# Optimization experiments

Measured on AMD Instinct MI355X. Metric: run time of the kernel, lower is better.

## Reference

```python
import jax, jax.numpy as jnp
import numpy as np

B, S, H, K = 32, 128, 512, 8  # batch, max_sentence_size, hidden_size, cross_share_k


def setup_inputs() -> dict:
    key = jax.random.key(0)
    ks = jax.random.split(key, 6)
    return {
        "aspect_hidden": jax.random.normal(ks[0], (B, S, H), jnp.float32),
        "polarity_hidden": jax.random.normal(ks[1], (B, S, H), jnp.float32),
        "G_aspect_polarity": jax.random.normal(ks[2], (H, K, H), jnp.float32) * 0.05,
        "G_polarity_aspect": jax.random.normal(ks[3], (H, K, H), jnp.float32) * 0.05,
        "G_vector_aspect": jax.random.normal(ks[4], (K, 1), jnp.float32),
        "G_vector_polarity": jax.random.normal(ks[5], (K, 1), jnp.float32),
    }


def _bilinear_score(left, G, right, v):
    # left:[B,S,H], G:[H,K,H], right:[B,T,H], v:[K,1] -> score:[B,S,T]
    # proj[b,s,k,g] = sum_h left[b,s,h] G[h,k,g]
    proj = jnp.einsum('bsh,hkg->bskg', left, G)
    # raw[b,s,t,k] = tanh(sum_g proj[b,s,k,g] right[b,t,g])  (matches source's
    # reshape->matmul->transpose chain)
    raw = jnp.tanh(jnp.einsum('bskg,btg->bstk', proj, right))
    return jnp.einsum('bstk,k->bst', raw, v[:, 0])


def reference(aspect_hidden, polarity_hidden, G_aspect_polarity,
              G_polarity_aspect, G_vector_aspect, G_vector_polarity):
    # Aspect branch: aspect x G_ap x polarity
    aspect_vector = _bilinear_score(aspect_hidden, G_aspect_polarity,
                                    polarity_hidden, G_vector_aspect)
    # Polarity branch: NOTE source uses aspect_hidden on BOTH sides (faithful)
    polarity_vector = _bilinear_score(aspect_hidden, G_polarity_aspect,
                                      aspect_hidden, G_vector_polarity)

    aspect_attn = jax.nn.softmax(aspect_vector, axis=-1)     # [B,S,S]
    polarity_attn = jax.nn.softmax(polarity_vector, axis=-1)  # [B,S,S]

    aspect_out = aspect_hidden + jnp.einsum('bst,bth->bsh', aspect_attn, polarity_hidden)
    polarity_out = polarity_hidden + jnp.einsum('bst,bth->bsh', polarity_attn, aspect_hidden)
    return (aspect_out, polarity_out)
```

## Files before the change

### kernel.cpp

```cpp
#include <hip/hip_runtime.h>

#define BB 32
#define SS 128
#define HH 512
#define KC 8
#define NN 4096

typedef __attribute__((ext_vector_type(8))) short bf16x8;
typedef __attribute__((ext_vector_type(8))) _Float16 f16x8;
typedef __attribute__((ext_vector_type(4))) float f32x4;

__device__ __forceinline__ unsigned short f2bf(float f) {
  unsigned int u = __float_as_uint(f);
  u += 0x7fffu + ((u >> 16) & 1u);
  return (unsigned short)(u >> 16);
}
__device__ __forceinline__ float bf2f(unsigned short h) {
  return __uint_as_float(((unsigned int)h) << 16);
}
__device__ __forceinline__ unsigned short f2fp16(float f) {
  union { _Float16 h; unsigned short u; } cv;
  cv.h = (_Float16)f;
  return cv.u;
}
__device__ __forceinline__ float tanh_fast(float x) {
  float e = __expf(2.0f * x);
  return 1.0f - 2.0f / (e + 1.0f);
}
__device__ __forceinline__ void async16(const void* g, void* lds) {
  __builtin_amdgcn_global_load_lds(
      (const __attribute__((address_space(1))) unsigned int*)g,
      (__attribute__((address_space(3))) unsigned int*)lds, 16, 0, 0);
}

__global__ __launch_bounds__(256) void convert_all(
    const float* __restrict__ Xa, const float* __restrict__ Xb,
    unsigned short* __restrict__ hia, unsigned short* __restrict__ loa,
    unsigned short* __restrict__ hiTa,
    unsigned short* __restrict__ hib, unsigned short* __restrict__ lob,
    unsigned short* __restrict__ hiTb,
    unsigned short* __restrict__ af16,
    const float* __restrict__ Ga, const float* __restrict__ Gb,
    unsigned short* __restrict__ g1f, unsigned short* __restrict__ g2f) {
  __shared__ float t[32][33];
  const int idx = blockIdx.x;
  const int tx = threadIdx.x & 31, ty = threadIdx.x >> 5;
  if (idx < 4096) {
    const int z = idx >> 11, rem = idx & 2047;
    const int h0 = (rem & 15) * 32;
    const int y = rem >> 4;
    const int s0 = (y & 3) * 32;
    const size_t b = y >> 2;
    const float* X = z ? Xb : Xa;
    unsigned short* hi = z ? hib : hia;
    unsigned short* lo = z ? lob : loa;
    unsigned short* hiT = z ? hiTb : hiTa;
#pragma unroll
    for (int r = 0; r < 4; ++r) {
      float f = X[b * (SS * HH) + (size_t)(s0 + ty + r * 8) * HH + h0 + tx];
      t[ty + r * 8][tx] = f;
      size_t o = b * (SS * HH) + (size_t)(s0 + ty + r * 8) * HH + h0 + tx;
      unsigned short h = f2bf(f);
      hi[o] = h;
      lo[o] = f2bf(f - bf2f(h));
      if (!z) af16[o] = f2fp16(f);
    }
    __syncthreads();
#pragma unroll
    for (int r = 0; r < 4; ++r) {
      float f = t[tx][ty + r * 8];
      size_t o = b * (SS * HH) + (size_t)(h0 + ty + r * 8) * SS + s0 + tx;
      hiT[o] = f2fp16(f);
    }
  } else {
    const int j = idx - 4096;
    const int z = j >> 11, rem = j & 2047;
    const int bx = (rem & 127) * 32;
    const int by = (rem >> 7) * 32;
    const float* G = z ? Gb : Ga;
    unsigned short* gf = z ? g2f : g1f;
#pragma unroll
    for (int r = 0; r < 4; ++r)
      t[ty + r * 8][tx] = G[(size_t)(by + ty + r * 8) * NN + bx + tx];
    __syncthreads();
#pragma unroll
    for (int r = 0; r < 4; ++r) {
      float f = t[tx][ty + r * 8];
      size_t o = (size_t)(bx + ty + r * 8) * HH + by + tx;
      gf[o] = f2fp16(f);
    }
  }
}

__global__ __launch_bounds__(256, 2) void fused_score(
    const unsigned short* __restrict__ Ahi, const unsigned short* __restrict__ Alo,
    const unsigned short* __restrict__ Phi, const unsigned short* __restrict__ Plo,
    const unsigned short* __restrict__ Af16,
    const unsigned short* __restrict__ G1f, const unsigned short* __restrict__ G2f,
    const float* __restrict__ v1, const float* __restrict__ v2,
    float* __restrict__ scoreBuf, int bc) {
  __shared__ __align__(16) char smem[65536];
  const int k = blockIdx.x;
  const int b = blockIdx.y;
  const int brx = blockIdx.z;
  const int tid = threadIdx.x, w = tid >> 6, L = tid & 63;
  const int wm = w >> 1, wn = w & 1;
  const int q = L >> 4, c = L & 15;

  const unsigned short* Af = Af16 + (size_t)b * SS * HH;
  const unsigned short* Gf = brx ? G2f : G1f;
  const unsigned short* Rh = (brx ? Ahi : Phi) + (size_t)b * SS * HH;
  const unsigned short* Rl = (brx ? Alo : Plo) + (size_t)b * SS * HH;

  const int rrA = L >> 3;
  const int scA = ((L & 7) ^ rrA) * 8;
  const unsigned short* pAf = Af + (size_t)(w * 32 + rrA) * HH + scA;
  const unsigned short* pGf = Gf + (size_t)(w * 32 + rrA) * HH + scA;

  const int srow = w * 32 + (L >> 2);
  const int slotS = ((L & 3) ^ ((L >> 3) & 3)) * 8;
  const unsigned short* pRh = Rh + (size_t)srow * HH + slotS;
  const unsigned short* pRl = Rl + (size_t)srow * HH + slotS;
  const unsigned lbase = (unsigned)w * 2048;

  const int xr = ((L & 15) >> 1) & 3;
  const int rslot = ((q ^ xr) << 4);
  const int arB = (wm * 64 + (L & 15)) * 64 + rslot;
  const int brB = (wn * 64 + (L & 15)) * 64 + rslot;

  f32x4 raw[4][4];
#pragma unroll
  for (int i = 0; i < 4; ++i)
#pragma unroll
    for (int j = 0; j < 4; ++j) raw[i][j] = (f32x4)(0.0f);

  auto stageA = [&](int gc, int ks, int buf) {
    const int k0 = ks * 64;
    const size_t n0 = (size_t)k * 512 + (size_t)gc * 128;
    char* bb = smem + buf * 32768;
#pragma unroll
    for (int c8 = 0; c8 < 4; ++c8) {
      async16(pAf + (size_t)(c8 * 8) * HH + k0, bb + w * 4096 + c8 * 1024);
      async16(pGf + (n0 + c8 * 8) * HH + k0, bb + 16384 + w * 4096 + c8 * 1024);
    }
  };

  auto stageR = [&](int gc, int sl, int buf) {
    const int gg = gc * 128 + sl * 32;
    char* bb = smem + buf * 32768;
    async16(pRh + gg, bb + 16384 + lbase);
    async16(pRh + gg + 16 * HH, bb + 16384 + lbase + 1024);
    async16(pRl + gg, bb + 24576 + lbase);
    async16(pRl + gg + 16 * HH, bb + 24576 + lbase + 1024);
  };

  auto computeA = [&](f32x4 (&acc)[4][4], int buf) {
    const char* bb = smem + buf * 32768;
    f16x8 ah[4][2], bh[4][2];
#pragma unroll
    for (int i = 0; i < 4; ++i) {
      const int R = wm * 64 + i * 16 + (L & 15);
#pragma unroll
      for (int kk = 0; kk < 2; ++kk) {
        const int sl8 = (kk * 4 + q) ^ (L & 7);
        ah[i][kk] = *(const f16x8*)(bb + R * 128 + sl8 * 16);
      }
    }
#pragma unroll
    for (int j = 0; j < 4; ++j) {
      const int Rb = wn * 64 + j * 16 + (L & 15);
#pragma unroll
      for (int kk = 0; kk < 2; ++kk) {
        const int sl8 = (kk * 4 + q) ^ (L & 7);
        bh[j][kk] = *(const f16x8*)(bb + 16384 + Rb * 128 + sl8 * 16);
      }
    }
    __builtin_amdgcn_s_setprio(1);
#pragma unroll
    for (int i = 0; i < 4; ++i)
#pragma unroll
      for (int j = 0; j < 4; ++j) {
        acc[i][j] = __builtin_amdgcn_mfma_f32_16x16x32_f16(ah[i][0], bh[j][0], acc[i][j], 0, 0, 0);
        acc[i][j] = __builtin_amdgcn_mfma_f32_16x16x32_f16(ah[i][1], bh[j][1], acc[i][j], 0, 0, 0);
      }
    __builtin_amdgcn_s_setprio(0);
  };

  auto computeB = [&](int buf) {
    const char* bb = smem + buf * 32768;
    bf16x8 sah[4], sal[4], sbh[4], sbl[4];
#pragma unroll
    for (int i = 0; i < 4; ++i) {
      sah[i] = *(const bf16x8*)(bb + arB + i * 1024);
      sal[i] = *(const bf16x8*)(bb + 8192 + arB + i * 1024);
    }
#pragma unroll
    for (int j = 0; j < 4; ++j) {
      sbh[j] = *(const bf16x8*)(bb + 16384 + brB + j * 1024);
      sbl[j] = *(const bf16x8*)(bb + 24576 + brB + j * 1024);
    }
    __builtin_amdgcn_s_setprio(1);
#pragma unroll
    for (int i = 0; i < 4; ++i)
#pragma unroll
      for (int j = 0; j < 4; ++j) {
        raw[i][j] = __builtin_amdgcn_mfma_f32_16x16x32_bf16(sah[i], sbh[j], raw[i][j], 0, 0, 0);
        raw[i][j] = __builtin_amdgcn_mfma_f32_16x16x32_bf16(sah[i], sbl[j], raw[i][j], 0, 0, 0);
        raw[i][j] = __builtin_amdgcn_mfma_f32_16x16x32_bf16(sal[i], sbh[j], raw[i][j], 0, 0, 0);
      }
    __builtin_amdgcn_s_setprio(0);
  };

  auto writeProj = [&](const f32x4 (&acc)[4][4], int sl, int buf) {
    if (wn == (sl >> 1)) {
      const int jj0 = (sl & 1) * 2;
      unsigned short* ph = (unsigned short*)(smem + buf * 32768);
      unsigned short* pl = ph + 4096;
#pragma unroll
      for (int i = 0; i < 4; ++i)
#pragma unroll
        for (int jd = 0; jd < 2; ++jd) {
          f32x4 vfr = acc[i][jj0 + jd];
#pragma unroll
          for (int r = 0; r < 4; ++r) {
            const int row = wm * 64 + i * 16 + q * 4 + r;
            const int gl = jd * 16 + c;
            const int ad = row * 32 + ((((gl >> 3) ^ ((row >> 1) & 3)) << 3)) + (gl & 7);
            float f = vfr[r];
            unsigned short h = f2bf(f);
            ph[ad] = h;
            pl[ad] = f2bf(f - bf2f(h));
          }
        }
    }
  };

  stageA(0, 0, 0);
  __syncthreads();

  for (int gc = 0; gc < 4; ++gc) {
    f32x4 acc[4][4];
#pragma unroll
    for (int i = 0; i < 4; ++i)
#pragma unroll
      for (int j = 0; j < 4; ++j) acc[i][j] = (f32x4)(0.0f);

    for (int ks = 0; ks < 7; ++ks) {
      stageA(gc, ks + 1, (ks + 1) & 1);
      computeA(acc, ks & 1);
      __syncthreads();
    }
    stageR(gc, 0, 0);
    computeA(acc, 1);
    writeProj(acc, 0, 0);
    __syncthreads();

#pragma unroll
    for (int sl = 0; sl < 4; ++sl) {
      if (sl < 3) stageR(gc, sl + 1, (sl + 1) & 1);
      else if (gc < 3) stageA(gc + 1, 0, 0);
      computeB(sl & 1);
      if (sl < 3) writeProj(acc, sl + 1, (sl + 1) & 1);
      __syncthreads();
    }
  }

  const float vk = (brx ? v2 : v1)[k];
  float* dst = scoreBuf + (((size_t)brx * bc + b) * KC + k) * (SS * SS);
#pragma unroll
  for (int i = 0; i < 4; ++i)
#pragma unroll
    for (int j = 0; j < 4; ++j) {
      const int row0 = wm * 64 + i * 16 + q * 4;
      const int col = wn * 64 + j * 16 + c;
#pragma unroll
      for (int r = 0; r < 4; ++r)
        dst[(size_t)(row0 + r) * SS + col] = vk * tanh_fast(raw[i][j][r]);
    }
}

__global__ __launch_bounds__(256) void softmax_attn(
    const float* __restrict__ scoreBuf, unsigned short* __restrict__ attnW) {
  const int x = blockIdx.x, rt = blockIdx.y;
  const int tid = threadIdx.x, tx = tid & 15, ty = tid >> 4;
  const size_t rowoff = (size_t)(rt * 16 + ty) * SS + tx * 8;
  const float* src = scoreBuf + (size_t)x * KC * (SS * SS) + rowoff;
  float sc[8];
#pragma unroll
  for (int j = 0; j < 8; ++j) sc[j] = 0.0f;
#pragma unroll
  for (int k = 0; k < KC; ++k) {
    float4 a0 = *(const float4*)&src[(size_t)k * (SS * SS)];
    float4 a1 = *(const float4*)&src[(size_t)k * (SS * SS) + 4];
    sc[0] += a0.x; sc[1] += a0.y; sc[2] += a0.z; sc[3] += a0.w;
    sc[4] += a1.x; sc[5] += a1.y; sc[6] += a1.z; sc[7] += a1.w;
  }
  float mx = sc[0];
#pragma unroll
  for (int j = 1; j < 8; ++j) mx = fmaxf(mx, sc[j]);
#pragma unroll
  for (int off = 1; off < 16; off <<= 1) mx = fmaxf(mx, __shfl_xor(mx, off, 16));
  float p[8], ssum = 0.0f;
#pragma unroll
  for (int j = 0; j < 8; ++j) { p[j] = __expf(sc[j] - mx); ssum += p[j]; }
#pragma unroll
  for (int off = 1; off < 16; off <<= 1) ssum += __shfl_xor(ssum, off, 16);
  float inv = 1.0f / ssum;
  ushort4 h0, h1;
  h0.x = f2fp16(p[0] * inv); h0.y = f2fp16(p[1] * inv);
  h0.z = f2fp16(p[2] * inv); h0.w = f2fp16(p[3] * inv);
  h1.x = f2fp16(p[4] * inv); h1.y = f2fp16(p[5] * inv);
  h1.z = f2fp16(p[6] * inv); h1.w = f2fp16(p[7] * inv);
  size_t abase = (size_t)x * (SS * SS) + rowoff;
  *(ushort4*)&attnW[abase] = h0;
  *(ushort4*)&attnW[abase + 4] = h1;
}

__global__ __launch_bounds__(256) void pv_res2(
    const unsigned short* __restrict__ attnW,
    const unsigned short* __restrict__ PTf, const unsigned short* __restrict__ ATf,
    const float* __restrict__ Abase, const float* __restrict__ Pbase,
    float* __restrict__ out1, float* __restrict__ out2, int bc) {
  __shared__ char smem[12288];
  unsigned short* sm = (unsigned short*)smem;
  const int x = blockIdx.x;
  const int brx = (x >= bc) ? 1 : 0;
  const int b = x - (brx ? bc : 0);
  const int hc = blockIdx.y & 3, sh = blockIdx.y >> 2;
  const int tid = threadIdx.x, w = tid >> 6, L = tid & 63;
  const int wm = w >> 1, wn = w & 1;

  const unsigned short* Aw = attnW + (size_t)x * (SS * SS) + (size_t)(sh * 64) * SS;
  const unsigned short* Vh = (brx ? ATf : PTf) + (size_t)b * HH * SS + (size_t)(hc * 128) * SS;
  const float* base = (brx ? Pbase : Abase) + (size_t)b * SS * HH;
  float* outp = (brx ? out2 : out1) + (size_t)b * SS * HH;

  f32x4 acc[2][4];
#pragma unroll
  for (int i = 0; i < 2; ++i)
#pragma unroll
    for (int j = 0; j < 4; ++j) acc[i][j] = (f32x4)(0.0f);

  const int arow = w * 16 + (L >> 2);
  const int brow = w * 32 + (L >> 2);
  const int scol = (L & 3) * 8;
  const int afr = (wm * 32 + (L & 15)) * 32 + (L >> 4) * 8;
  const int bfr = 2048 + (wn * 64 + (L & 15)) * 32 + (L >> 4) * 8;

  for (int kt = 0; kt < 4; ++kt) {
    const int k0 = kt * 32;
    async16(Aw + (size_t)arow * SS + k0 + scol, smem + w * 1024);
    async16(Vh + (size_t)brow * SS + k0 + scol, smem + 4096 + w * 2048);
    async16(Vh + (size_t)(brow + 16) * SS + k0 + scol, smem + 4096 + w * 2048 + 1024);
    __syncthreads();
    f16x8 af[2], bf[4];
#pragma unroll
    for (int i = 0; i < 2; ++i) af[i] = *(const f16x8*)&sm[afr + i * 512];
#pragma unroll
    for (int j = 0; j < 4; ++j) bf[j] = *(const f16x8*)&sm[bfr + j * 512];
#pragma unroll
    for (int i = 0; i < 2; ++i)
#pragma unroll
      for (int j = 0; j < 4; ++j)
        acc[i][j] = __builtin_amdgcn_mfma_f32_16x16x32_f16(af[i], bf[j], acc[i][j], 0, 0, 0);
    __syncthreads();
  }

  const int q = L >> 4, c = L & 15;
#pragma unroll
  for (int i = 0; i < 2; ++i)
#pragma unroll
    for (int j = 0; j < 4; ++j) {
      const int srow = sh * 64 + wm * 32 + i * 16 + q * 4;
      const int hcol = hc * 128 + wn * 64 + j * 16 + c;
#pragma unroll
      for (int r = 0; r < 4; ++r) {
        size_t o = (size_t)(srow + r) * HH + hcol;
        outp[o] = base[o] + acc[i][j][r];
      }
    }
}

extern "C" void kernel_launch(void* const* d_in, const int* in_sizes, int n_in,
                              void* d_out, int out_size, void* d_ws, size_t ws_size,
                              hipStream_t stream) {
  const float* A  = (const float*)d_in[0];
  const float* P  = (const float*)d_in[1];
  const float* G1 = (const float*)d_in[2];
  const float* G2 = (const float*)d_in[3];
  const float* v1 = (const float*)d_in[4];
  const float* v2 = (const float*)d_in[5];
  float* out1 = (float*)d_out;
  float* out2 = out1 + (size_t)BB * SS * HH;

  const size_t NA = (size_t)BB * SS * HH;
  const size_t NG = (size_t)HH * KC * HH;
  unsigned short* Ahi = (unsigned short*)d_ws;
  unsigned short* Alo = Ahi + NA;
  unsigned short* Phi = Alo + NA;
  unsigned short* Plo = Phi + NA;
  unsigned short* Af16 = Plo + NA;
  unsigned short* G1f = Af16 + NA;
  unsigned short* G2f = G1f + NG;
  unsigned short* ATf = G2f + NG;
  unsigned short* PTf = ATf + NA;

  const size_t fixedBytes = (7 * NA + 2 * NG) * sizeof(unsigned short);
  const size_t perB = 2 * (size_t)SS * SS * (KC * sizeof(float) + sizeof(unsigned short));
  size_t rem = ws_size > fixedBytes ? ws_size - fixedBytes : 0;
  int Bc = (int)(rem / perB);
  if (Bc < 1) Bc = 1;
  if (Bc > BB) Bc = BB;
  float* scoreBuf = (float*)((char*)d_ws + fixedBytes);
  unsigned short* attnW = (unsigned short*)(scoreBuf + 2 * (size_t)Bc * KC * SS * SS);

  convert_all<<<dim3(8192), 256, 0, stream>>>(
      A, P, Ahi, Alo, ATf, Phi, Plo, PTf, Af16, G1, G2, G1f, G2f);

  for (int b0 = 0; b0 < BB; b0 += Bc) {
    int bc = (Bc < BB - b0) ? Bc : (BB - b0);
    size_t off = (size_t)b0 * SS * HH;
    fused_score<<<dim3(KC, bc, 2), 256, 0, stream>>>(
        Ahi + off, Alo + off, Phi + off, Plo + off, Af16 + off,
        G1f, G2f, v1, v2, scoreBuf, bc);
    softmax_attn<<<dim3(bc * 2, 8), 256, 0, stream>>>(scoreBuf, attnW);
    pv_res2<<<dim3(bc * 2, 8), 256, 0, stream>>>(
        attnW, PTf + off, ATf + off, A + off, P + off,
        out1 + off, out2 + off, bc);
  }
}
```

Before: 221.9 us.

## Replace split-bf16 second GEMM with single fp16 MFMA and fp16 score buffer

The second bilinear GEMM (proj x right) used a three-term hi/lo bf16 split to approximate fp32 accuracy. It now uses one fp16 MFMA with fp16 operands, so the lo/hi conversion passes and their workspace buffers go away. The per-k score buffer is also stored as fp16 instead of fp32, halving that write and read traffic between the score and softmax kernels. The cost is lower precision in the tanh inputs and scores, which may push error close to the tolerance.

Measured after the change: 182.2 us. 17.9% less time.

```diff
diff --git a/kernel.cpp b/kernel.cpp
--- a/kernel.cpp
+++ b/kernel.cpp
@@ -6,18 +6,9 @@
 #define KC 8
 #define NN 4096
 
-typedef __attribute__((ext_vector_type(8))) short bf16x8;
 typedef __attribute__((ext_vector_type(8))) _Float16 f16x8;
 typedef __attribute__((ext_vector_type(4))) float f32x4;
 
-__device__ __forceinline__ unsigned short f2bf(float f) {
-  unsigned int u = __float_as_uint(f);
-  u += 0x7fffu + ((u >> 16) & 1u);
-  return (unsigned short)(u >> 16);
-}
-__device__ __forceinline__ float bf2f(unsigned short h) {
-  return __uint_as_float(((unsigned int)h) << 16);
-}
 __device__ __forceinline__ unsigned short f2fp16(float f) {
   union { _Float16 h; unsigned short u; } cv;
   cv.h = (_Float16)f;
@@ -35,11 +26,8 @@
 
 __global__ __launch_bounds__(256) void convert_all(
     const float* __restrict__ Xa, const float* __restrict__ Xb,
-    unsigned short* __restrict__ hia, unsigned short* __restrict__ loa,
-    unsigned short* __restrict__ hiTa,
-    unsigned short* __restrict__ hib, unsigned short* __restrict__ lob,
-    unsigned short* __restrict__ hiTb,
-    unsigned short* __restrict__ af16,
+    unsigned short* __restrict__ af16, unsigned short* __restrict__ pf16,
+    unsigned short* __restrict__ aT16, unsigned short* __restrict__ pT16,
     const float* __restrict__ Ga, const float* __restrict__ Gb,
     unsigned short* __restrict__ g1f, unsigned short* __restrict__ g2f) {
   __shared__ float t[32][33];
@@ -52,25 +40,21 @@
     const int s0 = (y & 3) * 32;
     const size_t b = y >> 2;
     const float* X = z ? Xb : Xa;
-    unsigned short* hi = z ? hib : hia;
-    unsigned short* lo = z ? lob : loa;
-    unsigned short* hiT = z ? hiTb : hiTa;
+    unsigned short* xf = z ? pf16 : af16;
+    unsigned short* xT = z ? pT16 : aT16;
 #pragma unroll
     for (int r = 0; r < 4; ++r) {
       float f = X[b * (SS * HH) + (size_t)(s0 + ty + r * 8) * HH + h0 + tx];
       t[ty + r * 8][tx] = f;
       size_t o = b * (SS * HH) + (size_t)(s0 + ty + r * 8) * HH + h0 + tx;
-      unsigned short h = f2bf(f);
-      hi[o] = h;
-      lo[o] = f2bf(f - bf2f(h));
-      if (!z) af16[o] = f2fp16(f);
+      xf[o] = f2fp16(f);
     }
     __syncthreads();
 #pragma unroll
     for (int r = 0; r < 4; ++r) {
       float f = t[tx][ty + r * 8];
       size_t o = b * (SS * HH) + (size_t)(h0 + ty + r * 8) * SS + s0 + tx;
-      hiT[o] = f2fp16(f);
+      xT[o] = f2fp16(f);
     }
   } else {
     const int j = idx - 4096;
@@ -93,12 +77,10 @@
 }
 
 __global__ __launch_bounds__(256, 2) void fused_score(
-    const unsigned short* __restrict__ Ahi, const unsigned short* __restrict__ Alo,
-    const unsigned short* __restrict__ Phi, const unsigned short* __restrict__ Plo,
-    const unsigned short* __restrict__ Af16,
+    const unsigned short* __restrict__ Af16, const unsigned short* __restrict__ Pf16,
     const unsigned short* __restrict__ G1f, const unsigned short* __restrict__ G2f,
     const float* __restrict__ v1, const float* __restrict__ v2,
-    float* __restrict__ scoreBuf, int bc) {
+    unsigned short* __restrict__ scoreH, int bc) {
   __shared__ __align__(16) char smem[65536];
   const int k = blockIdx.x;
   const int b = blockIdx.y;
@@ -109,8 +91,7 @@
 
   const unsigned short* Af = Af16 + (size_t)b * SS * HH;
   const unsigned short* Gf = brx ? G2f : G1f;
-  const unsigned short* Rh = (brx ? Ahi : Phi) + (size_t)b * SS * HH;
-  const unsigned short* Rl = (brx ? Alo : Plo) + (size_t)b * SS * HH;
+  const unsigned short* Rf = (brx ? Af16 : Pf16) + (size_t)b * SS * HH;
 
   const int rrA = L >> 3;
   const int scA = ((L & 7) ^ rrA) * 8;
@@ -119,8 +100,7 @@
 
   const int srow = w * 32 + (L >> 2);
   const int slotS = ((L & 3) ^ ((L >> 3) & 3)) * 8;
-  const unsigned short* pRh = Rh + (size_t)srow * HH + slotS;
-  const unsigned short* pRl = Rl + (size_t)srow * HH + slotS;
+  const unsigned short* pRf = Rf + (size_t)srow * HH + slotS;
   const unsigned lbase = (unsigned)w * 2048;
 
   const int xr = ((L & 15) >> 1) & 3;
@@ -148,10 +128,8 @@
   auto stageR = [&](int gc, int sl, int buf) {
     const int gg = gc * 128 + sl * 32;
     char* bb = smem + buf * 32768;
-    async16(pRh + gg, bb + 16384 + lbase);
-    async16(pRh + gg + 16 * HH, bb + 16384 + lbase + 1024);
-    async16(pRl + gg, bb + 24576 + lbase);
-    async16(pRl + gg + 16 * HH, bb + 24576 + lbase + 1024);
+    async16(pRf + gg, bb + 16384 + lbase);
+    async16(pRf + gg + 16 * HH, bb + 16384 + lbase + 1024);
   };
 
   auto computeA = [&](f32x4 (&acc)[4][4], int buf) {
@@ -188,26 +166,19 @@
 
   auto computeB = [&](int buf) {
     const char* bb = smem + buf * 32768;
-    bf16x8 sah[4], sal[4], sbh[4], sbl[4];
-#pragma unroll
-    for (int i = 0; i < 4; ++i) {
-      sah[i] = *(const bf16x8*)(bb + arB + i * 1024);
-      sal[i] = *(const bf16x8*)(bb + 8192 + arB + i * 1024);
-    }
-#pragma unroll
-    for (int j = 0; j < 4; ++j) {
-      sbh[j] = *(const bf16x8*)(bb + 16384 + brB + j * 1024);
-      sbl[j] = *(const bf16x8*)(bb + 24576 + brB + j * 1024);
-    }
+    f16x8 sa[4], sb[4];
+#pragma unroll
+    for (int i = 0; i < 4; ++i)
+      sa[i] = *(const f16x8*)(bb + arB + i * 1024);
+#pragma unroll
+    for (int j = 0; j < 4; ++j)
+      sb[j] = *(const f16x8*)(bb + 16384 + brB + j * 1024);
     __builtin_amdgcn_s_setprio(1);
 #pragma unroll
     for (int i = 0; i < 4; ++i)
 #pragma unroll
-      for (int j = 0; j < 4; ++j) {
-        raw[i][j] = __builtin_amdgcn_mfma_f32_16x16x32_bf16(sah[i], sbh[j], raw[i][j], 0, 0, 0);
-        raw[i][j] = __builtin_amdgcn_mfma_f32_16x16x32_bf16(sah[i], sbl[j], raw[i][j], 0, 0, 0);
-        raw[i][j] = __builtin_amdgcn_mfma_f32_16x16x32_bf16(sal[i], sbh[j], raw[i][j], 0, 0, 0);
-      }
+      for (int j = 0; j < 4; ++j)
+        raw[i][j] = __builtin_amdgcn_mfma_f32_16x16x32_f16(sa[i], sb[j], raw[i][j], 0, 0, 0);
     __builtin_amdgcn_s_setprio(0);
   };
 
@@ -215,7 +186,6 @@
     if (wn == (sl >> 1)) {
       const int jj0 = (sl & 1) * 2;
       unsigned short* ph = (unsigned short*)(smem + buf * 32768);
-      unsigned short* pl = ph + 4096;
 #pragma unroll
       for (int i = 0; i < 4; ++i)
 #pragma unroll
@@ -226,10 +196,7 @@
             const int row = wm * 64 + i * 16 + q * 4 + r;
             const int gl = jd * 16 + c;
             const int ad = row * 32 + ((((gl >> 3) ^ ((row >> 1) & 3)) << 3)) + (gl & 7);
-            float f = vfr[r];
-            unsigned short h = f2bf(f);
-            ph[ad] = h;
-            pl[ad] = f2bf(f - bf2f(h));
+            ph[ad] = f2fp16(vfr[r]);
           }
         }
     }
@@ -266,7 +233,7 @@
   }
 
   const float vk = (brx ? v2 : v1)[k];
-  float* dst = scoreBuf + (((size_t)brx * bc + b) * KC + k) * (SS * SS);
+  unsigned short* dst = scoreH + (((size_t)brx * bc + b) * KC + k) * (SS * SS);
 #pragma unroll
   for (int i = 0; i < 4; ++i)
 #pragma unroll
@@ -275,25 +242,24 @@
       const int col = wn * 64 + j * 16 + c;
 #pragma unroll
       for (int r = 0; r < 4; ++r)
-        dst[(size_t)(row0 + r) * SS + col] = vk * tanh_fast(raw[i][j][r]);
+        dst[(size_t)(row0 + r) * SS + col] = f2fp16(vk * tanh_fast(raw[i][j][r]));
     }
 }
 
 __global__ __launch_bounds__(256) void softmax_attn(
-    const float* __restrict__ scoreBuf, unsigned short* __restrict__ attnW) {
+    const unsigned short* __restrict__ scoreH, unsigned short* __restrict__ attnW) {
   const int x = blockIdx.x, rt = blockIdx.y;
   const int tid = threadIdx.x, tx = tid & 15, ty = tid >> 4;
   const size_t rowoff = (size_t)(rt * 16 + ty) * SS + tx * 8;
-  const float* src = scoreBuf + (size_t)x * KC * (SS * SS) + rowoff;
+  const unsigned short* src = scoreH + (size_t)x * KC * (SS * SS) + rowoff;
   float sc[8];
 #pragma unroll
   for (int j = 0; j < 8; ++j) sc[j] = 0.0f;
 #pragma unroll
   for (int k = 0; k < KC; ++k) {
-    float4 a0 = *(const float4*)&src[(size_t)k * (SS * SS)];
-    float4 a1 = *(const float4*)&src[(size_t)k * (SS * SS) + 4];
-    sc[0] += a0.x; sc[1] += a0.y; sc[2] += a0.z; sc[3] += a0.w;
-    sc[4] += a1.x; sc[5] += a1.y; sc[6] += a1.z; sc[7] += a1.w;
+    f16x8 a = *(const f16x8*)&src[(size_t)k * (SS * SS)];
+#pragma unroll
+    for (int j = 0; j < 8; ++j) sc[j] += (float)a[j];
   }
   float mx = sc[0];
 #pragma unroll
@@ -395,35 +361,32 @@
 
   const size_t NA = (size_t)BB * SS * HH;
   const size_t NG = (size_t)HH * KC * HH;
-  unsigned short* Ahi = (unsigned short*)d_ws;
-  unsigned short* Alo = Ahi + NA;
-  unsigned short* Phi = Alo + NA;
-  unsigned short* Plo = Phi + NA;
-  unsigned short* Af16 = Plo + NA;
-  unsigned short* G1f = Af16 + NA;
+  unsigned short* Af16 = (unsigned short*)d_ws;
+  unsigned short* Pf16 = Af16 + NA;
+  unsigned short* G1f = Pf16 + NA;
   unsigned short* G2f = G1f + NG;
   unsigned short* ATf = G2f + NG;
   unsigned short* PTf = ATf + NA;
 
-  const size_t fixedBytes = (7 * NA + 2 * NG) * sizeof(unsigned short);
-  const size_t perB = 2 * (size_t)SS * SS * (KC * sizeof(float) + sizeof(unsigned short));
+  const size_t fixedBytes = (4 * NA + 2 * NG) * sizeof(unsigned short);
+  const size_t perB = 2 * (size_t)SS * SS *
+                      (KC * sizeof(unsigned short) + sizeof(unsigned short));
   size_t rem = ws_size > fixedBytes ? ws_size - fixedBytes : 0;
   int Bc = (int)(rem / perB);
   if (Bc < 1) Bc = 1;
   if (Bc > BB) Bc = BB;
-  float* scoreBuf = (float*)((char*)d_ws + fixedBytes);
-  unsigned short* attnW = (unsigned short*)(scoreBuf + 2 * (size_t)Bc * KC * SS * SS);
+  unsigned short* scoreH = (unsigned short*)((char*)d_ws + fixedBytes);
+  unsigned short* attnW = scoreH + 2 * (size_t)Bc * KC * SS * SS;
 
   convert_all<<<dim3(8192), 256, 0, stream>>>(
-      A, P, Ahi, Alo, ATf, Phi, Plo, PTf, Af16, G1, G2, G1f, G2f);
+      A, P, Af16, Pf16, ATf, PTf, G1, G2, G1f, G2f);
 
   for (int b0 = 0; b0 < BB; b0 += Bc) {
     int bc = (Bc < BB - b0) ? Bc : (BB - b0);
     size_t off = (size_t)b0 * SS * HH;
     fused_score<<<dim3(KC, bc, 2), 256, 0, stream>>>(
-        Ahi + off, Alo + off, Phi + off, Plo + off, Af16 + off,
-        G1f, G2f, v1, v2, scoreBuf, bc);
-    softmax_attn<<<dim3(bc * 2, 8), 256, 0, stream>>>(scoreBuf, attnW);
+        Af16 + off, Pf16 + off, G1f, G2f, v1, v2, scoreH, bc);
+    softmax_attn<<<dim3(bc * 2, 8), 256, 0, stream>>>(scoreH, attnW);
     pv_res2<<<dim3(bc * 2, 8), 256, 0, stream>>>(
         attnW, PTf + off, ATf + off, A + off, P + off,
         out1 + off, out2 + off, bc);
```
